# Kernel optimization log

Measured on AMD Instinct MI355X. Metric: run time of the kernel, lower is better.

The kernel has to match this reference:

```python
import jax, jax.numpy as jnp
import numpy as np

HIDDEN = 1024
FFN = 3584
NUM_EXPERTS = 8
TOP_K = 2
B, S = 2, 1024


def setup_inputs() -> dict:
    key = jax.random.key(0)
    k0, k1, k2, k3 = jax.random.split(key, 4)
    hidden_states = jax.random.normal(k0, (B, S, HIDDEN), dtype=jnp.float32)
    # torch Linear stores [out, in]; we keep gate as [E, H] (matches nn.Linear weight)
    gate_w = jax.random.normal(k1, (NUM_EXPERTS, HIDDEN), dtype=jnp.float32) * 0.02
    # GroupedLinear weights stored as [E, in, out] for direct x @ W per expert
    w_gate_up = jax.random.normal(k2, (NUM_EXPERTS, HIDDEN, 2 * FFN), dtype=jnp.float32) * 0.02
    w_down = jax.random.normal(k3, (NUM_EXPERTS, FFN, HIDDEN), dtype=jnp.float32) * 0.02
    return {"hidden_states": hidden_states, "gate_w": gate_w,
            "w_gate_up": w_gate_up, "w_down": w_down}


def reference(hidden_states, gate_w, w_gate_up, w_down):
    b, s, h = hidden_states.shape
    x = hidden_states.reshape(-1, h)                      # [T, H]
    T = x.shape[0]
    E = gate_w.shape[0]

    # Router: logits -> fp32 softmax -> top-k -> renormalize (Mixtral semantics)
    router_logits = x @ gate_w.T                          # [T, E]
    probs = jax.nn.softmax(router_logits.astype(jnp.float32), axis=-1)
    top_vals, top_idx = jax.lax.top_k(probs, TOP_K)       # [T, K]
    top_vals = top_vals / top_vals.sum(axis=-1, keepdims=True)
    top_vals = top_vals.astype(x.dtype)

    # Dense combine weights [T, E]: scatter top-k probs to expert slots.
    # Equivalent to permute -> grouped GEMM -> unpermute-with-probs.
    combine = jnp.zeros((T, E), dtype=x.dtype).at[
        jnp.arange(T)[:, None], top_idx].add(top_vals)

    out = jnp.zeros_like(x)
    for e in range(E):  # fixed small expert count
        gu = x @ w_gate_up[e]                             # [T, 2F]
        gate_proj, up_proj = jnp.split(gu, 2, axis=-1)
        act = jax.nn.silu(gate_proj) * up_proj            # [T, F]
        out = out + combine[:, e:e + 1] * (act @ w_down[e])

    return out.reshape(b, s, h), router_logits
```

## Files before the change

kernel.cpp:

```cpp
#include <hip/hip_runtime.h>
#include <hip/hip_bf16.h>
#include <stdint.h>

#define HIDDEN  1024
#define FFN     3584
#define NE      8
#define NTOK    2048
#define CAP     2048
#define OUT_ELEMS (NTOK * HIDDEN)

#define X_OFF    0u
#define CNT_OFF  (4u*1024u*1024u)
#define TOK_OFF  (CNT_OFF + 256u)
#define WGT_OFF  (TOK_OFF + 65536u)
#define INV_OFF  (WGT_OFF + 65536u)
#define ACT_OFF  (INV_OFF + 16384u)
#define ACT_SZ   (4096u * 3584u * 2u)
#define WGU_OFF  (ACT_OFF + ACT_SZ)
#define WGU_SZ   (8u*56u*16u*16384u)
#define WDB_OFF  (WGU_OFF + WGU_SZ)
#define WDB_SZ   (8u*8u*56u*16384u)
#define PART_OFF (WDB_OFF + WDB_SZ)
#define PART_SZ  (4096u*1024u*4u)
#define WS_NEED  ((size_t)PART_OFF + (size_t)PART_SZ)

typedef __attribute__((ext_vector_type(8))) short short8;
typedef __attribute__((ext_vector_type(4))) float floatx4;

static __device__ __forceinline__ uint32_t f2bf(float f) {
  union { float f; uint32_t u; } v; v.f = f;
  return (v.u + 0x7FFFu + ((v.u >> 16) & 1u)) >> 16;
}
static __device__ __forceinline__ uint32_t pack2(float lo, float hi) {
  return f2bf(lo) | (f2bf(hi) << 16);
}
union S8U { uint4 u; short8 s; };
static __device__ __forceinline__ short8 as_short8(uint4 v) { S8U x; x.u = v; return x.s; }

static __device__ __forceinline__ void ld_g2l16(const void* g, void* l) {
  __builtin_amdgcn_global_load_lds(
      (const __attribute__((address_space(1))) void*)g,
      (__attribute__((address_space(3))) void*)l, 16, 0, 0);
}

static __device__ __forceinline__ void stage_tile(
    const char* const* aptr, const char* bptr, size_t akt, size_t bkt,
    uint4* AsB, uint4* BsB, int w)
{
#pragma unroll
  for (int it = 0; it < 4; ++it)
    ld_g2l16(aptr[it] + akt, &AsB[(w * 4 + it) * 64]);
#pragma unroll
  for (int it = 0; it < 4; ++it)
    ld_g2l16(bptr + bkt + (size_t)it * 1024u, &BsB[(w * 4 + it) * 64]);
}

#define WAIT_VM8()  do { __builtin_amdgcn_sched_barrier(0); \
                         asm volatile("s_waitcnt vmcnt(8)" ::: "memory"); } while (0)
#define WAIT_VM0()  do { __builtin_amdgcn_sched_barrier(0); \
                         asm volatile("s_waitcnt vmcnt(0)" ::: "memory"); } while (0)
#define BAR()       do { __builtin_amdgcn_s_barrier(); \
                         __builtin_amdgcn_sched_barrier(0); } while (0)
#define ENDBAR()    do { __builtin_amdgcn_sched_barrier(0); \
                         __builtin_amdgcn_s_barrier(); } while (0)

__global__ __launch_bounds__(256) void moe_prep(float4* __restrict__ out4,
                                                int* __restrict__ cnt) {
  uint32_t i = blockIdx.x * 256u + threadIdx.x;
  out4[i] = make_float4(0.f, 0.f, 0.f, 0.f);
  if (blockIdx.x == 0 && threadIdx.x < NE) cnt[threadIdx.x] = 0;
}

__global__ __launch_bounds__(256) void moe_convert(const float4* __restrict__ x4,
                                                   uint4* __restrict__ xb,
                                                   int* __restrict__ cnt) {
  uint32_t g = blockIdx.x * 256u + threadIdx.x;
  float4 a = x4[2u*g], b = x4[2u*g + 1u];
  xb[g] = make_uint4(pack2(a.x, a.y), pack2(a.z, a.w),
                     pack2(b.x, b.y), pack2(b.z, b.w));
  if (blockIdx.x == 0 && threadIdx.x < NE) cnt[threadIdx.x] = 0;
}

__global__ __launch_bounds__(256) void moe_router(
    const float* __restrict__ x, const float* __restrict__ gw,
    float* __restrict__ logits, int* __restrict__ cnt,
    int* __restrict__ tok, float* __restrict__ wgt, int* __restrict__ inv)
{
  const int t = blockIdx.x * 4 + (threadIdx.x >> 6);
  const int lane = threadIdx.x & 63;
  const float* xr = x + (size_t)t * HIDDEN;
  float a[NE];
#pragma unroll
  for (int e = 0; e < NE; ++e) a[e] = 0.f;
  for (int hh = 0; hh < HIDDEN / 64; ++hh) {
    float xv = xr[hh * 64 + lane];
#pragma unroll
    for (int e = 0; e < NE; ++e) a[e] += xv * gw[e * HIDDEN + hh * 64 + lane];
  }
#pragma unroll
  for (int off = 32; off > 0; off >>= 1) {
#pragma unroll
    for (int e = 0; e < NE; ++e) a[e] += __shfl_xor(a[e], off);
  }
  if (lane == 0) {
#pragma unroll
    for (int e = 0; e < NE; ++e) logits[t * NE + e] = a[e];
    int i0 = 0; float v0 = a[0];
#pragma unroll
    for (int e = 1; e < NE; ++e) if (a[e] > v0) { v0 = a[e]; i0 = e; }
    int i1 = (i0 == 0) ? 1 : 0; float v1 = a[i1];
#pragma unroll
    for (int e = 0; e < NE; ++e) if (e != i0 && a[e] > v1) { v1 = a[e]; i1 = e; }
    float w0 = 1.f / (1.f + __expf(v1 - v0));
    float w1 = 1.f - w0;
    int p0 = atomicAdd(&cnt[i0], 1); tok[i0 * CAP + p0] = t; wgt[i0 * CAP + p0] = w0;
    int p1 = atomicAdd(&cnt[i1], 1); tok[i1 * CAP + p1] = t; wgt[i1 * CAP + p1] = w1;
    inv[t * 2 + 0] = i0 * CAP + p0;
    inv[t * 2 + 1] = i1 * CAP + p1;
  }
}

__global__ __launch_bounds__(256) void moe_wconv_gu(const float* __restrict__ wgu,
                                                    uint4* __restrict__ wgub) {
  const int kt = blockIdx.x, fb = blockIdx.y, e = blockIdx.z;
  const int f0 = fb * 64, k0 = kt * 64;
  const float* wB = wgu + (size_t)e * HIDDEN * (2 * FFN);
  uint4* dst = wgub + ((size_t)(e * 56 + fb) * 16 + kt) * 1024;

  __shared__ float lds_f[64 * 129];

#pragma unroll
  for (int p = 0; p < 8; ++p) {
    int idx = p * 256 + threadIdx.x;
    int r   = idx >> 5;
    int lc  = (idx & 31) * 4;
    int col = f0 + ((lc >> 6) << 5) + (lc & 31) + (((lc >> 5) & 1) ? FFN : 0);
    float4 v = *(const float4*)(wB + (size_t)(k0 + r) * (2 * FFN) + col);
    float* d = &lds_f[r * 129 + lc];
    d[0] = v.x; d[1] = v.y; d[2] = v.z; d[3] = v.w;
  }
  __syncthreads();
#pragma unroll
  for (int p = 0; p < 4; ++p) {
    int m  = p * 256 + threadIdx.x;
    int ne = m >> 3, c8 = m & 7;
    float f[8];
#pragma unroll
    for (int kk = 0; kk < 8; ++kk) f[kk] = lds_f[(c8 * 8 + kk) * 129 + ne];
    dst[ne * 8 + (c8 ^ (ne & 7))] =
        make_uint4(pack2(f[0], f[1]), pack2(f[2], f[3]),
                   pack2(f[4], f[5]), pack2(f[6], f[7]));
  }
}

__global__ __launch_bounds__(256) void moe_wconv_d(const float* __restrict__ wd,
                                                   uint4* __restrict__ wdb) {
  const int kt = blockIdx.x, nb = blockIdx.y, e = blockIdx.z;
  const int n0 = nb * 128, k0 = kt * 64;
  const float* wB = wd + (size_t)e * FFN * HIDDEN;
  uint4* dst = wdb + ((size_t)(e * 8 + nb) * 56 + kt) * 1024;

  __shared__ float lds_f[64 * 129];

#pragma unroll
  for (int p = 0; p < 8; ++p) {
    int idx = p * 256 + threadIdx.x;
    int r   = idx >> 5;
    int lc  = (idx & 31) * 4;
    float4 v = *(const float4*)(wB + (size_t)(k0 + r) * HIDDEN + n0 + lc);
    float* d = &lds_f[r * 129 + lc];
    d[0] = v.x; d[1] = v.y; d[2] = v.z; d[3] = v.w;
  }
  __syncthreads();
#pragma unroll
  for (int p = 0; p < 4; ++p) {
    int m  = p * 256 + threadIdx.x;
    int ne = m >> 3, c8 = m & 7;
    float f[8];
#pragma unroll
    for (int kk = 0; kk < 8; ++kk) f[kk] = lds_f[(c8 * 8 + kk) * 129 + ne];
    dst[ne * 8 + (c8 ^ (ne & 7))] =
        make_uint4(pack2(f[0], f[1]), pack2(f[2], f[3]),
                   pack2(f[4], f[5]), pack2(f[6], f[7]));
  }
}

__global__ __launch_bounds__(256) void moe_gateup(
    const uint4* __restrict__ xb, const uint4* __restrict__ wgub,
    const int* __restrict__ cnt, const int* __restrict__ tok,
    unsigned short* __restrict__ act)
{
  const int e  = blockIdx.z;
  const int m0 = blockIdx.y * 128;
  const int fb = blockIdx.x;
  const int f0 = fb * 64;
  const int cn = cnt[e];
  if (m0 >= cn) return;
  int basev = 0;
#pragma unroll
  for (int i = 0; i < NE; ++i) { int ci = cnt[i]; if (i < e) basev += ci; }

  __shared__ uint4 As[2][1024];
  __shared__ uint4 Bs4[2][1024];

  const int tid  = threadIdx.x;
  const int lane = tid & 63;
  const int w    = tid >> 6;
  const int wm   = w >> 1, wn = w & 1;
  const int q    = lane >> 4;
  const int c    = lane & 15;

  const int* tokE = tok + e * CAP;
  const char* aptr[4];
#pragma unroll
  for (int it = 0; it < 4; ++it) {
    int p   = (w * 4 + it) * 64 + lane;
    int row = p >> 3, c8 = p & 7;
    int mrow = m0 + row; if (mrow >= cn) mrow = cn - 1;
    aptr[it] = (const char*)(xb + (size_t)tokE[mrow] * (HIDDEN / 8) + (c8 ^ (row & 7)));
  }
  const char* bptr = (const char*)wgub + ((size_t)(e * 56 + fb) * 16) * 16384u
                   + (size_t)w * 4096u + (size_t)lane * 16u;

  floatx4 acc[4][4];
#pragma unroll
  for (int i = 0; i < 4; ++i)
#pragma unroll
    for (int j = 0; j < 4; ++j) acc[i][j] = (floatx4){0.f, 0.f, 0.f, 0.f};

  const int NT = HIDDEN / 64;
  stage_tile(aptr, bptr, 0, 0, As[0], Bs4[0], w);
  int cur = 0;
  for (int kt = 0; kt < NT; ++kt) {
    if (kt + 1 < NT) {
      stage_tile(aptr, bptr, (size_t)(kt + 1) * 128u, (size_t)(kt + 1) * 16384u,
                 As[cur ^ 1], Bs4[cur ^ 1], w);
      WAIT_VM8();
    } else {
      WAIT_VM0();
    }
    BAR();
    const uint4* Asc = As[cur];
    const uint4* Bsc = Bs4[cur];
#pragma unroll
    for (int ks = 0; ks < 2; ++ks) {
      const int kc8 = ks * 4 + q;
      short8 af[4];
#pragma unroll
      for (int i = 0; i < 4; ++i) {
        int row = wm * 64 + i * 16 + c;
        af[i] = as_short8(Asc[row * 8 + (kc8 ^ (row & 7))]);
      }
      short8 bfr[4];
#pragma unroll
      for (int j = 0; j < 4; ++j) {
        int n = wn * 64 + j * 16 + c;
        bfr[j] = as_short8(Bsc[n * 8 + (kc8 ^ (n & 7))]);
      }
#pragma unroll
      for (int i = 0; i < 4; ++i)
#pragma unroll
        for (int j = 0; j < 4; ++j)
          acc[i][j] = __builtin_amdgcn_mfma_f32_16x16x32_bf16(af[i], bfr[j], acc[i][j], 0, 0, 0);
    }
    ENDBAR();
    cur ^= 1;
  }

#pragma unroll
  for (int i = 0; i < 4; ++i) {
#pragma unroll
    for (int r = 0; r < 4; ++r) {
      int m = m0 + wm * 64 + i * 16 + q * 4 + r;
      if (m < cn) {
#pragma unroll
        for (int j = 0; j < 2; ++j) {
          float g = acc[i][j][r];
          float u = acc[i][j + 2][r];
          float a = (g / (1.f + __expf(-g))) * u;
          act[(size_t)(basev + m) * FFN + (f0 + wn * 32 + j * 16 + c)] = (unsigned short)f2bf(a);
        }
      }
    }
  }
}

__global__ __launch_bounds__(256) void moe_down(
    const unsigned short* __restrict__ act, const uint4* __restrict__ wdb,
    const int* __restrict__ cnt, const int* __restrict__ tok,
    const float* __restrict__ wgt, float* __restrict__ part)
{
  const int e  = blockIdx.z;
  const int m0 = blockIdx.y * 128;
  const int nb = blockIdx.x;
  const int n0 = nb * 128;
  const int cn = cnt[e];
  if (m0 >= cn) return;
  int basev = 0;
#pragma unroll
  for (int i = 0; i < NE; ++i) { int ci = cnt[i]; if (i < e) basev += ci; }

  __shared__ uint4 As[2][1024];
  __shared__ uint4 Bs4[2][1024];

  const int tid  = threadIdx.x;
  const int lane = tid & 63;
  const int w    = tid >> 6;
  const int wm   = w >> 1, wn = w & 1;
  const int q    = lane >> 4;
  const int c    = lane & 15;

  const char* aptr[4];
#pragma unroll
  for (int it = 0; it < 4; ++it) {
    int p   = (w * 4 + it) * 64 + lane;
    int row = p >> 3, c8 = p & 7;
    int mrow = m0 + row; if (mrow >= cn) mrow = cn - 1;
    aptr[it] = (const char*)act +
               ((size_t)(basev + mrow) * FFN + (size_t)((c8 ^ (row & 7)) * 8)) * 2u;
  }
  const char* bptr = (const char*)wdb + ((size_t)(e * 8 + nb) * 56) * 16384u
                   + (size_t)w * 4096u + (size_t)lane * 16u;

  floatx4 acc[4][4];
#pragma unroll
  for (int i = 0; i < 4; ++i)
#pragma unroll
    for (int j = 0; j < 4; ++j) acc[i][j] = (floatx4){0.f, 0.f, 0.f, 0.f};

  const int NT = FFN / 64;
  stage_tile(aptr, bptr, 0, 0, As[0], Bs4[0], w);
  int cur = 0;
  for (int kt = 0; kt < NT; ++kt) {
    if (kt + 1 < NT) {
      stage_tile(aptr, bptr, (size_t)(kt + 1) * 128u, (size_t)(kt + 1) * 16384u,
                 As[cur ^ 1], Bs4[cur ^ 1], w);
      WAIT_VM8();
    } else {
      WAIT_VM0();
    }
    BAR();
    const uint4* Asc = As[cur];
    const uint4* Bsc = Bs4[cur];
#pragma unroll
    for (int ks = 0; ks < 2; ++ks) {
      const int kc8 = ks * 4 + q;
      short8 af[4];
#pragma unroll
      for (int i = 0; i < 4; ++i) {
        int row = wm * 64 + i * 16 + c;
        af[i] = as_short8(Asc[row * 8 + (kc8 ^ (row & 7))]);
      }
      short8 bfr[4];
#pragma unroll
      for (int j = 0; j < 4; ++j) {
        int n = wn * 64 + j * 16 + c;
        bfr[j] = as_short8(Bsc[n * 8 + (kc8 ^ (n & 7))]);
      }
#pragma unroll
      for (int i = 0; i < 4; ++i)
#pragma unroll
        for (int j = 0; j < 4; ++j)
          acc[i][j] = __builtin_amdgcn_mfma_f32_16x16x32_bf16(af[i], bfr[j], acc[i][j], 0, 0, 0);
    }
    ENDBAR();
    cur ^= 1;
  }

#pragma unroll
  for (int i = 0; i < 4; ++i) {
#pragma unroll
    for (int r = 0; r < 4; ++r) {
      int m = m0 + wm * 64 + i * 16 + q * 4 + r;
      if (m < cn) {
        float  wg   = wgt[e * CAP + m];
        float* prow = part + (size_t)(basev + m) * HIDDEN + n0 + wn * 64 + c;
#pragma unroll
        for (int j = 0; j < 4; ++j)
          prow[j * 16] = acc[i][j][r] * wg;
      }
    }
  }
}

__global__ __launch_bounds__(256) void moe_combine(
    const int* __restrict__ cnt, const int* __restrict__ inv,
    const float4* __restrict__ part4, float4* __restrict__ out4)
{
  const int t  = blockIdx.x;
  const int s0 = inv[2 * t], s1 = inv[2 * t + 1];
  const int e0 = s0 >> 11, e1 = s1 >> 11;
  int b0 = 0, b1 = 0;
#pragma unroll
  for (int i = 0; i < NE; ++i) {
    int ci = cnt[i];
    if (i < e0) b0 += ci;
    if (i < e1) b1 += ci;
  }
  const size_t r0 = (size_t)(b0 + (s0 & (CAP - 1))) * 256u;
  const size_t r1 = (size_t)(b1 + (s1 & (CAP - 1))) * 256u;
  const int i = threadIdx.x;
  float4 a = part4[r0 + i];
  float4 b = part4[r1 + i];
  out4[(size_t)t * 256u + i] = make_float4(a.x + b.x, a.y + b.y, a.z + b.z, a.w + b.w);
}

__global__ __launch_bounds__(256) void moe_gateup_lg(
    const uint4* __restrict__ xb, const float* __restrict__ wgu,
    const int* __restrict__ cnt, const int* __restrict__ tok,
    unsigned short* __restrict__ act)
{
  const int e  = blockIdx.z;
  const int m0 = blockIdx.y * 128;
  const int f0 = blockIdx.x * 64;
  const int cn = cnt[e];
  if (m0 >= cn) return;
  int basev = 0;
#pragma unroll
  for (int i = 0; i < NE; ++i) { int ci = cnt[i]; if (i < e) basev += ci; }

  __shared__ uint4    As[1024];
  __shared__ uint32_t Bs[4096];

  const int tid  = threadIdx.x;
  const int lane = tid & 63;
  const int w    = tid >> 6;
  const int wm   = w >> 1, wn = w & 1;
  const int q    = lane >> 4;
  const int c    = lane & 15;

  floatx4 acc[4][4];
#pragma unroll
  for (int i = 0; i < 4; ++i)
#pragma unroll
    for (int j = 0; j < 4; ++j) acc[i][j] = (floatx4){0.f, 0.f, 0.f, 0.f};

  const float* wB  = wgu + (size_t)e * HIDDEN * (2 * FFN);
  const int* tokE  = tok + e * CAP;

  for (int kt = 0; kt < HIDDEN / 64; ++kt) {
    const int k0 = kt * 64;
    __syncthreads();
#pragma unroll
    for (int it = 0; it < 4; ++it) {
      int cid = it * 256 + tid;
      int row = cid >> 3, c8 = cid & 7;
      int mrow = m0 + row; if (mrow >= cn) mrow = cn - 1;
      int tk = tokE[mrow];
      As[row * 8 + (c8 ^ (row & 7))] = xb[(size_t)tk * (HIDDEN / 8) + (k0 >> 3) + c8];
    }
#pragma unroll
    for (int it = 0; it < 4; ++it) {
      int mid = it * 256 + tid;
      int kp = mid >> 5;
      int n  = (mid & 31) * 4;
      int col = f0 + ((n >> 6) << 5) + (n & 31) + (((n >> 5) & 1) ? FFN : 0);
      const float* src = wB + (size_t)(k0 + 2 * kp) * (2 * FFN) + col;
      float4 r0 = *(const float4*)src;
      float4 r1 = *(const float4*)(src + 2 * FFN);
      int widx = kp * 128 + (n ^ (((kp >> 2) & 1) << 4));
      *(uint4*)&Bs[widx] = make_uint4(pack2(r0.x, r1.x), pack2(r0.y, r1.y),
                                      pack2(r0.z, r1.z), pack2(r0.w, r1.w));
    }
    __syncthreads();
#pragma unroll
    for (int ks = 0; ks < 2; ++ks) {
      short8 af[4];
#pragma unroll
      for (int i = 0; i < 4; ++i) {
        int row = wm * 64 + i * 16 + c;
        int kc8 = ks * 4 + q;
        af[i] = as_short8(As[row * 8 + (kc8 ^ (row & 7))]);
      }
      short8 bfr[4];
#pragma unroll
      for (int j = 0; j < 4; ++j) {
        int n  = wn * 64 + j * 16 + c;
        int kp = ks * 16 + q * 4;
        int nn = n ^ ((q & 1) << 4);
        bfr[j] = as_short8(make_uint4(Bs[(kp + 0) * 128 + nn], Bs[(kp + 1) * 128 + nn],
                                      Bs[(kp + 2) * 128 + nn], Bs[(kp + 3) * 128 + nn]));
      }
#pragma unroll
      for (int i = 0; i < 4; ++i)
#pragma unroll
        for (int j = 0; j < 4; ++j)
          acc[i][j] = __builtin_amdgcn_mfma_f32_16x16x32_bf16(af[i], bfr[j], acc[i][j], 0, 0, 0);
    }
  }

#pragma unroll
  for (int i = 0; i < 4; ++i) {
#pragma unroll
    for (int r = 0; r < 4; ++r) {
      int m = m0 + wm * 64 + i * 16 + q * 4 + r;
      if (m < cn) {
#pragma unroll
        for (int j = 0; j < 2; ++j) {
          float g = acc[i][j][r];
          float u = acc[i][j + 2][r];
          float a = (g / (1.f + __expf(-g))) * u;
          act[(size_t)(basev + m) * FFN + (f0 + wn * 32 + j * 16 + c)] = (unsigned short)f2bf(a);
        }
      }
    }
  }
}

__global__ __launch_bounds__(256) void moe_down_lg(
    const uint4* __restrict__ actc, const float* __restrict__ wd,
    const int* __restrict__ cnt, const int* __restrict__ tok,
    const float* __restrict__ wgt, float* __restrict__ out)
{
  const int e  = blockIdx.z;
  const int m0 = blockIdx.y * 128;
  const int n0 = blockIdx.x * 128;
  const int cn = cnt[e];
  if (m0 >= cn) return;
  int basev = 0;
#pragma unroll
  for (int i = 0; i < NE; ++i) { int ci = cnt[i]; if (i < e) basev += ci; }

  __shared__ uint4    As[1024];
  __shared__ uint32_t Bs[4096];

  const int tid  = threadIdx.x;
  const int lane = tid & 63;
  const int w    = tid >> 6;
  const int wm   = w >> 1, wn = w & 1;
  const int q    = lane >> 4;
  const int c    = lane & 15;

  floatx4 acc[4][4];
#pragma unroll
  for (int i = 0; i < 4; ++i)
#pragma unroll
    for (int j = 0; j < 4; ++j) acc[i][j] = (floatx4){0.f, 0.f, 0.f, 0.f};

  const float* wB = wd + (size_t)e * FFN * HIDDEN;

  for (int kt = 0; kt < FFN / 64; ++kt) {
    const int k0 = kt * 64;
    __syncthreads();
#pragma unroll
    for (int it = 0; it < 4; ++it) {
      int cid = it * 256 + tid;
      int row = cid >> 3, c8 = cid & 7;
      int mrow = m0 + row; if (mrow >= cn) mrow = cn - 1;
      As[row * 8 + (c8 ^ (row & 7))] =
          actc[(size_t)(basev + mrow) * (FFN / 8) + (k0 >> 3) + c8];
    }
#pragma unroll
    for (int it = 0; it < 4; ++it) {
      int mid = it * 256 + tid;
      int kp = mid >> 5;
      int n  = (mid & 31) * 4;
      int col = n0 + n;
      const float* src = wB + (size_t)(k0 + 2 * kp) * HIDDEN + col;
      float4 r0 = *(const float4*)src;
      float4 r1 = *(const float4*)(src + HIDDEN);
      int widx = kp * 128 + (n ^ (((kp >> 2) & 1) << 4));
      *(uint4*)&Bs[widx] = make_uint4(pack2(r0.x, r1.x), pack2(r0.y, r1.y),
                                      pack2(r0.z, r1.z), pack2(r0.w, r1.w));
    }
    __syncthreads();
#pragma unroll
    for (int ks = 0; ks < 2; ++ks) {
      short8 af[4];
#pragma unroll
      for (int i = 0; i < 4; ++i) {
        int row = wm * 64 + i * 16 + c;
        int kc8 = ks * 4 + q;
        af[i] = as_short8(As[row * 8 + (kc8 ^ (row & 7))]);
      }
      short8 bfr[4];
#pragma unroll
      for (int j = 0; j < 4; ++j) {
        int n  = wn * 64 + j * 16 + c;
        int kp = ks * 16 + q * 4;
        int nn = n ^ ((q & 1) << 4);
        bfr[j] = as_short8(make_uint4(Bs[(kp + 0) * 128 + nn], Bs[(kp + 1) * 128 + nn],
                                      Bs[(kp + 2) * 128 + nn], Bs[(kp + 3) * 128 + nn]));
      }
#pragma unroll
      for (int i = 0; i < 4; ++i)
#pragma unroll
        for (int j = 0; j < 4; ++j)
          acc[i][j] = __builtin_amdgcn_mfma_f32_16x16x32_bf16(af[i], bfr[j], acc[i][j], 0, 0, 0);
    }
  }

#pragma unroll
  for (int i = 0; i < 4; ++i) {
#pragma unroll
    for (int r = 0; r < 4; ++r) {
      int m = m0 + wm * 64 + i * 16 + q * 4 + r;
      if (m < cn) {
        int   t  = tok[e * CAP + m];
        float wg = wgt[e * CAP + m];
        float* orow = out + (size_t)t * HIDDEN + n0 + wn * 64 + c;
#pragma unroll
        for (int j = 0; j < 4; ++j)
          atomicAdd(orow + j * 16, acc[i][j][r] * wg);
      }
    }
  }
}

extern "C" void kernel_launch(void* const* d_in, const int* in_sizes, int n_in,
                              void* d_out, int out_size, void* d_ws, size_t ws_size,
                              hipStream_t stream)
{
  (void)in_sizes; (void)n_in; (void)out_size;
  const float* x   = (const float*)d_in[0];
  const float* gw  = (const float*)d_in[1];
  const float* wgu = (const float*)d_in[2];
  const float* wd  = (const float*)d_in[3];
  float* out = (float*)d_out;
  char*  ws  = (char*)d_ws;

  uint4*          xb   = (uint4*)(ws + X_OFF);
  int*            cnt  = (int*)(ws + CNT_OFF);
  int*            tok  = (int*)(ws + TOK_OFF);
  float*          wgt  = (float*)(ws + WGT_OFF);
  int*            inv  = (int*)(ws + INV_OFF);
  unsigned short* act  = (unsigned short*)(ws + ACT_OFF);
  uint4*          wgub = (uint4*)(ws + WGU_OFF);
  uint4*          wdb  = (uint4*)(ws + WDB_OFF);
  float*          part = (float*)(ws + PART_OFF);

  const bool fast = (ws_size >= WS_NEED);

  if (fast) {
    moe_convert<<<(NTOK * HIDDEN) / (256 * 8), 256, 0, stream>>>((const float4*)x, xb, cnt);
    moe_router<<<NTOK / 4, 256, 0, stream>>>(x, gw, out + OUT_ELEMS, cnt, tok, wgt, inv);
    moe_wconv_gu<<<dim3(16, 56, NE), 256, 0, stream>>>(wgu, wgub);
    moe_wconv_d<<<dim3(56, 8, NE), 256, 0, stream>>>(wd, wdb);
    moe_gateup<<<dim3(FFN / 64, 16, NE), 256, 0, stream>>>(xb, wgub, cnt, tok, act);
    moe_down<<<dim3(HIDDEN / 128, 16, NE), 256, 0, stream>>>(act, wdb, cnt, tok, wgt, part);
    moe_combine<<<NTOK, 256, 0, stream>>>(cnt, inv, (const float4*)part, (float4*)out);
  } else {
    moe_prep<<<OUT_ELEMS / (256 * 4), 256, 0, stream>>>((float4*)out, cnt);
    moe_convert<<<(NTOK * HIDDEN) / (256 * 8), 256, 0, stream>>>((const float4*)x, xb, cnt);
    moe_router<<<NTOK / 4, 256, 0, stream>>>(x, gw, out + OUT_ELEMS, cnt, tok, wgt, inv);
    moe_gateup_lg<<<dim3(FFN / 64, 16, NE), 256, 0, stream>>>(xb, wgu, cnt, tok, act);
    moe_down_lg<<<dim3(HIDDEN / 128, 16, NE), 256, 0, stream>>>((const uint4*)act, wd, cnt, tok, wgt, out);
  }
}
```

Baseline: 659.6 us.

## Fuse gate/up weight conversion into the gate-up GEMM with larger M tiles

Removes the separate fp32-to-bf16 conversion pass for the gate/up weights. The gate-up GEMM now reads fp32 weights directly, converts them in registers and writes them swizzled into LDS. The block grows to 512 threads covering 512 token rows, so each converted weight tile is reused across four times more rows. The A/B LDS double buffering is replaced by a single buffer with register prefetch of the next weight tile, which may expose more load latency. Register pressure also rises with 32 accumulators per wave.

```diff
diff --git a/kernel.cpp b/kernel.cpp
--- a/kernel.cpp
+++ b/kernel.cpp
@@ -56,9 +56,15 @@
 }
 
 #define WAIT_VM8()  do { __builtin_amdgcn_sched_barrier(0); \
-                         asm volatile("s_waitcnt vmcnt(8)" ::: "memory"); } while (0)
+                         asm volatile("s_waitcnt vmcnt(8)" ::: "memory"); \
+                         __builtin_amdgcn_sched_barrier(0); } while (0)
+#define WAIT_VM16() do { __builtin_amdgcn_sched_barrier(0); \
+                         asm volatile("s_waitcnt vmcnt(16)" ::: "memory"); \
+                         __builtin_amdgcn_sched_barrier(0); } while (0)
 #define WAIT_VM0()  do { __builtin_amdgcn_sched_barrier(0); \
-                         asm volatile("s_waitcnt vmcnt(0)" ::: "memory"); } while (0)
+                         asm volatile("s_waitcnt vmcnt(0)" ::: "memory"); \
+                         __builtin_amdgcn_sched_barrier(0); } while (0)
+#define WAIT_LGKM() do { asm volatile("s_waitcnt lgkmcnt(0)" ::: "memory"); } while (0)
 #define BAR()       do { __builtin_amdgcn_s_barrier(); \
                          __builtin_amdgcn_sched_barrier(0); } while (0)
 #define ENDBAR()    do { __builtin_amdgcn_sched_barrier(0); \
@@ -120,39 +126,6 @@
   }
 }
 
-__global__ __launch_bounds__(256) void moe_wconv_gu(const float* __restrict__ wgu,
-                                                    uint4* __restrict__ wgub) {
-  const int kt = blockIdx.x, fb = blockIdx.y, e = blockIdx.z;
-  const int f0 = fb * 64, k0 = kt * 64;
-  const float* wB = wgu + (size_t)e * HIDDEN * (2 * FFN);
-  uint4* dst = wgub + ((size_t)(e * 56 + fb) * 16 + kt) * 1024;
-
-  __shared__ float lds_f[64 * 129];
-
-#pragma unroll
-  for (int p = 0; p < 8; ++p) {
-    int idx = p * 256 + threadIdx.x;
-    int r   = idx >> 5;
-    int lc  = (idx & 31) * 4;
-    int col = f0 + ((lc >> 6) << 5) + (lc & 31) + (((lc >> 5) & 1) ? FFN : 0);
-    float4 v = *(const float4*)(wB + (size_t)(k0 + r) * (2 * FFN) + col);
-    float* d = &lds_f[r * 129 + lc];
-    d[0] = v.x; d[1] = v.y; d[2] = v.z; d[3] = v.w;
-  }
-  __syncthreads();
-#pragma unroll
-  for (int p = 0; p < 4; ++p) {
-    int m  = p * 256 + threadIdx.x;
-    int ne = m >> 3, c8 = m & 7;
-    float f[8];
-#pragma unroll
-    for (int kk = 0; kk < 8; ++kk) f[kk] = lds_f[(c8 * 8 + kk) * 129 + ne];
-    dst[ne * 8 + (c8 ^ (ne & 7))] =
-        make_uint4(pack2(f[0], f[1]), pack2(f[2], f[3]),
-                   pack2(f[4], f[5]), pack2(f[6], f[7]));
-  }
-}
-
 __global__ __launch_bounds__(256) void moe_wconv_d(const float* __restrict__ wd,
                                                    uint4* __restrict__ wdb) {
   const int kt = blockIdx.x, nb = blockIdx.y, e = blockIdx.z;
@@ -185,13 +158,13 @@
   }
 }
 
-__global__ __launch_bounds__(256) void moe_gateup(
-    const uint4* __restrict__ xb, const uint4* __restrict__ wgub,
+__global__ __launch_bounds__(512) void moe_gateup_f(
+    const uint4* __restrict__ xb, const float* __restrict__ wgu,
     const int* __restrict__ cnt, const int* __restrict__ tok,
     unsigned short* __restrict__ act)
 {
   const int e  = blockIdx.z;
-  const int m0 = blockIdx.y * 128;
+  const int m0 = blockIdx.y * 512;
   const int fb = blockIdx.x;
   const int f0 = fb * 64;
   const int cn = cnt[e];
@@ -200,85 +173,108 @@
 #pragma unroll
   for (int i = 0; i < NE; ++i) { int ci = cnt[i]; if (i < e) basev += ci; }
 
-  __shared__ uint4 As[2][1024];
-  __shared__ uint4 Bs4[2][1024];
+  __shared__ uint4 As[4096];
+  __shared__ uint4 Bs[1024];
 
   const int tid  = threadIdx.x;
   const int lane = tid & 63;
   const int w    = tid >> 6;
-  const int wm   = w >> 1, wn = w & 1;
   const int q    = lane >> 4;
   const int c    = lane & 15;
 
   const int* tokE = tok + e * CAP;
-  const char* aptr[4];
-#pragma unroll
-  for (int it = 0; it < 4; ++it) {
-    int p   = (w * 4 + it) * 64 + lane;
+  const char* aptr[8];
+#pragma unroll
+  for (int it = 0; it < 8; ++it) {
+    int p   = (w * 8 + it) * 64 + lane;
     int row = p >> 3, c8 = p & 7;
     int mrow = m0 + row; if (mrow >= cn) mrow = cn - 1;
     aptr[it] = (const char*)(xb + (size_t)tokE[mrow] * (HIDDEN / 8) + (c8 ^ (row & 7)));
   }
-  const char* bptr = (const char*)wgub + ((size_t)(e * 56 + fb) * 16) * 16384u
-                   + (size_t)w * 4096u + (size_t)lane * 16u;
-
-  floatx4 acc[4][4];
+
+  const int ne  = tid & 127;
+  const int c8b = tid >> 7;
+  const int col = f0 + ((ne >> 6) << 5) + (ne & 31) + (((ne >> 5) & 1) ? FFN : 0);
+  const float* colp = wgu + (size_t)e * HIDDEN * (2 * FFN) + col;
+  const int wi0 = ne * 8 + (c8b ^ (ne & 7));
+  const int wi1 = ne * 8 + ((c8b + 4) ^ (ne & 7));
+
+  floatx4 acc[4][8];
 #pragma unroll
   for (int i = 0; i < 4; ++i)
 #pragma unroll
-    for (int j = 0; j < 4; ++j) acc[i][j] = (floatx4){0.f, 0.f, 0.f, 0.f};
+    for (int j = 0; j < 8; ++j) acc[i][j] = (floatx4){0.f, 0.f, 0.f, 0.f};
+
+  float rv[16];
+#pragma unroll
+  for (int s = 0; s < 2; ++s)
+#pragma unroll
+    for (int kk = 0; kk < 8; ++kk)
+      rv[s * 8 + kk] = colp[(size_t)((c8b + 4 * s) * 8 + kk) * (2 * FFN)];
 
   const int NT = HIDDEN / 64;
-  stage_tile(aptr, bptr, 0, 0, As[0], Bs4[0], w);
-  int cur = 0;
   for (int kt = 0; kt < NT; ++kt) {
+    WAIT_VM0();
+    uint4 pk0 = make_uint4(pack2(rv[0], rv[1]),  pack2(rv[2], rv[3]),
+                           pack2(rv[4], rv[5]),  pack2(rv[6], rv[7]));
+    uint4 pk1 = make_uint4(pack2(rv[8], rv[9]),  pack2(rv[10], rv[11]),
+                           pack2(rv[12], rv[13]), pack2(rv[14], rv[15]));
+    Bs[wi0] = pk0;
+    Bs[wi1] = pk1;
+#pragma unroll
+    for (int it = 0; it < 8; ++it)
+      ld_g2l16(aptr[it] + (size_t)kt * 128u, &As[(w * 8 + it) * 64]);
     if (kt + 1 < NT) {
-      stage_tile(aptr, bptr, (size_t)(kt + 1) * 128u, (size_t)(kt + 1) * 16384u,
-                 As[cur ^ 1], Bs4[cur ^ 1], w);
-      WAIT_VM8();
+      const int kb = (kt + 1) * 64;
+#pragma unroll
+      for (int s = 0; s < 2; ++s)
+#pragma unroll
+        for (int kk = 0; kk < 8; ++kk)
+          rv[s * 8 + kk] = colp[(size_t)(kb + (c8b + 4 * s) * 8 + kk) * (2 * FFN)];
+      WAIT_VM16();
     } else {
       WAIT_VM0();
     }
+    WAIT_LGKM();
     BAR();
-    const uint4* Asc = As[cur];
-    const uint4* Bsc = Bs4[cur];
 #pragma unroll
     for (int ks = 0; ks < 2; ++ks) {
       const int kc8 = ks * 4 + q;
       short8 af[4];
 #pragma unroll
       for (int i = 0; i < 4; ++i) {
-        int row = wm * 64 + i * 16 + c;
-        af[i] = as_short8(Asc[row * 8 + (kc8 ^ (row & 7))]);
-      }
-      short8 bfr[4];
-#pragma unroll
-      for (int j = 0; j < 4; ++j) {
-        int n = wn * 64 + j * 16 + c;
-        bfr[j] = as_short8(Bsc[n * 8 + (kc8 ^ (n & 7))]);
+        int row = w * 64 + i * 16 + c;
+        af[i] = as_short8(As[row * 8 + (kc8 ^ (row & 7))]);
+      }
+      short8 bfr[8];
+#pragma unroll
+      for (int j = 0; j < 8; ++j) {
+        int n = j * 16 + c;
+        bfr[j] = as_short8(Bs[n * 8 + (kc8 ^ (n & 7))]);
       }
 #pragma unroll
       for (int i = 0; i < 4; ++i)
 #pragma unroll
-        for (int j = 0; j < 4; ++j)
+        for (int j = 0; j < 8; ++j)
           acc[i][j] = __builtin_amdgcn_mfma_f32_16x16x32_bf16(af[i], bfr[j], acc[i][j], 0, 0, 0);
     }
     ENDBAR();
-    cur ^= 1;
   }
 
 #pragma unroll
   for (int i = 0; i < 4; ++i) {
 #pragma unroll
     for (int r = 0; r < 4; ++r) {
-      int m = m0 + wm * 64 + i * 16 + q * 4 + r;
+      int m = m0 + w * 64 + i * 16 + q * 4 + r;
       if (m < cn) {
-#pragma unroll
-        for (int j = 0; j < 2; ++j) {
-          float g = acc[i][j][r];
-          float u = acc[i][j + 2][r];
+        unsigned short* arow = act + (size_t)(basev + m) * FFN;
+#pragma unroll
+        for (int t4 = 0; t4 < 4; ++t4) {
+          const int jj = (t4 & 1) | ((t4 >> 1) << 2);
+          float g = acc[i][jj][r];
+          float u = acc[i][jj + 2][r];
           float a = (g / (1.f + __expf(-g))) * u;
-          act[(size_t)(basev + m) * FFN + (f0 + wn * 32 + j * 16 + c)] = (unsigned short)f2bf(a);
+          arow[f0 + ((jj >> 2) << 5) + (jj & 1) * 16 + c] = (unsigned short)f2bf(a);
         }
       }
     }
@@ -625,7 +621,6 @@
   float*          wgt  = (float*)(ws + WGT_OFF);
   int*            inv  = (int*)(ws + INV_OFF);
   unsigned short* act  = (unsigned short*)(ws + ACT_OFF);
-  uint4*          wgub = (uint4*)(ws + WGU_OFF);
   uint4*          wdb  = (uint4*)(ws + WDB_OFF);
   float*          part = (float*)(ws + PART_OFF);
 
@@ -634,9 +629,8 @@
   if (fast) {
     moe_convert<<<(NTOK * HIDDEN) / (256 * 8), 256, 0, stream>>>((const float4*)x, xb, cnt);
     moe_router<<<NTOK / 4, 256, 0, stream>>>(x, gw, out + OUT_ELEMS, cnt, tok, wgt, inv);
-    moe_wconv_gu<<<dim3(16, 56, NE), 256, 0, stream>>>(wgu, wgub);
     moe_wconv_d<<<dim3(56, 8, NE), 256, 0, stream>>>(wd, wdb);
-    moe_gateup<<<dim3(FFN / 64, 16, NE), 256, 0, stream>>>(xb, wgub, cnt, tok, act);
+    moe_gateup_f<<<dim3(FFN / 64, CAP / 512, NE), 512, 0, stream>>>(xb, wgu, cnt, tok, act);
     moe_down<<<dim3(HIDDEN / 128, 16, NE), 256, 0, stream>>>(act, wdb, cnt, tok, wgt, part);
     moe_combine<<<NTOK, 256, 0, stream>>>(cnt, inv, (const float4*)part, (float4*)out);
   } else {
```

Result: faster. 626.5 us (-5.0%).
